# Kernel optimization log

Hardware: AMD Instinct MI355X
Metric: run time of the kernel (lower is better)

The kernel has to match this reference:

```python
import jax, jax.numpy as jnp
import numpy as np

N = 8192      # num nodes
D = 256       # input feature dim (num_embeddings)
F_OUT = 128   # out_channels
B = 4096      # lookup batch size


def setup_inputs() -> dict:
    key = jax.random.key(0)
    k1, k2, k3, k4 = jax.random.split(key, 4)
    x = jax.random.randint(k1, (B,), 0, N)                      # node ids for final lookup
    adj = jax.random.randint(k2, (N, N), 0, 2).astype(jnp.int32)  # dense 0/1 adjacency
    embedding = jax.random.normal(k3, (N, D), dtype=jnp.float32)
    xavier = 1.414 * (6.0 / (D + F_OUT)) ** 0.5
    W = jax.random.uniform(k4, (D, F_OUT), minval=-xavier, maxval=xavier, dtype=jnp.float32)
    return {"x": x, "adj": adj, "embedding": embedding, "W": W}


def reference(x, adj, embedding, W):
    Wh = embedding @ W                                   # [N, F_OUT]
    mask = adj > 0
    maskf = mask.astype(Wh.dtype)
    # per-row neighbor mean of Wh (vectorized form of the python row loop)
    deg = jnp.maximum(jnp.sum(maskf, axis=1), 1.0)       # guard; random adj has deg>0
    neigh_mean = (maskf @ Wh) / deg[:, None]             # [N, F_OUT]
    alpha = jnp.sum(Wh * neigh_mean, axis=1)             # [N], Wh[i] . mean(neighbors)
    e = Wh @ Wh.T + alpha[:, None]                       # similarity + row-wise query term
    att = jax.nn.softmax(jnp.where(mask, e, jnp.asarray(-9e15, e.dtype)), axis=1)
    # dropout is identity in eval mode (p effectively 0)
    h_prime = att @ Wh                                   # [N, F_OUT]
    emb_out = jax.nn.elu(h_prime)                        # concat=True branch
    out = emb_out[x]                                     # F.embedding lookup, [B, F_OUT]
    nrm = jnp.linalg.norm(out, axis=1, keepdims=True)
    return out / jnp.maximum(nrm, 1e-12)                 # F.normalize (L2, eps=1e-12)
```

## Files before the change

kernel.cpp:

```cpp
#include <hip/hip_runtime.h>

#define NN 8192
#define DD 256
#define FF 128
#define BB 4096
#define NSPLIT 16
#define KCHUNK (NN / NSPLIT)
#define NITER (KCHUNK / 64)

typedef unsigned short ushortT;
typedef __attribute__((ext_vector_type(8))) short bf16x8;
typedef __attribute__((ext_vector_type(4))) float f32x4;

__device__ __forceinline__ ushortT f2bf(float f) {
  unsigned u = __float_as_uint(f);
  return (ushortT)((u + 0x7FFFu + ((u >> 16) & 1u)) >> 16);
}
__device__ __forceinline__ float bf2f(ushortT h) {
  return __uint_as_float(((unsigned)h) << 16);
}


__global__ __launch_bounds__(256) void init_kernel(int* flags, int* cnt) {
  int i = blockIdx.x * 256 + threadIdx.x;
  flags[i] = 0;
  if (i == 0) *cnt = 0;
}

__global__ __launch_bounds__(256) void scatter_kernel(const int* __restrict__ x, int* flags) {
  int b = blockIdx.x * 256 + threadIdx.x;
  flags[x[b]] = 1;
}

__global__ __launch_bounds__(256) void compact_kernel(const int* __restrict__ flags, int* cnt,
                                                      int* list, int* slot) {
  int i = blockIdx.x * 256 + threadIdx.x;
  if (flags[i]) {
    int pos = atomicAdd(cnt, 1);
    list[pos] = i;
    slot[i] = pos;
  }
}


__global__ __launch_bounds__(256) void pack_kernel(const int* __restrict__ adj,
                                                   const int* __restrict__ list,
                                                   const int* __restrict__ cntp,
                                                   unsigned* __restrict__ pk) {
  const int s = blockIdx.x >> 2;
  const int kc = (blockIdx.x & 3) * 2048;
  if (s >= *cntp) return;
  const int w = threadIdx.x >> 6, l = threadIdx.x & 63;
  const int* base = adj + (size_t)list[s] * NN + kc + w * 512;
  unsigned long long* dst = (unsigned long long*)(pk + s * 256 + (kc >> 5) + w * 16);
#pragma unroll
  for (int i = 0; i < 8; ++i) {
    unsigned long long b = __ballot(base[i * 64 + l] > 0);
    if (l == 0) dst[i] = b;
  }
}


__global__ __launch_bounds__(256) void wh_kernel(const float* __restrict__ emb,
                                                 const float* __restrict__ W,
                                                 ushortT* __restrict__ Whh,
                                                 ushortT* __restrict__ Whl) {
  __shared__ float Es[32 * 65];
  __shared__ float Ws[64 * 128];
  const int t = threadIdx.x;
  const int r0 = blockIdx.x * 32;
  const int rg = t >> 5;
  const int cg = t & 31;
  float4 acc[4] = {{0,0,0,0},{0,0,0,0},{0,0,0,0},{0,0,0,0}};
  for (int kc = 0; kc < DD; kc += 64) {
    __syncthreads();
    for (int i = 0; i < 8; ++i) {
      int idx = t + 256 * i;
      int r = idx >> 6, k = idx & 63;
      Es[r * 65 + k] = emb[(r0 + r) * DD + kc + k];
    }
    for (int i = 0; i < 8; ++i) {
      int idx = t + 256 * i;
      int kr = idx >> 5, c4 = (idx & 31) * 4;
      *(float4*)&Ws[kr * 128 + c4] = *(const float4*)&W[(kc + kr) * 128 + c4];
    }
    __syncthreads();
    for (int k = 0; k < 64; ++k) {
      float4 b = *(const float4*)&Ws[k * 128 + cg * 4];
#pragma unroll
      for (int i = 0; i < 4; ++i) {
        float a = Es[(rg * 4 + i) * 65 + k];
        acc[i].x += a * b.x; acc[i].y += a * b.y;
        acc[i].z += a * b.z; acc[i].w += a * b.w;
      }
    }
  }
#pragma unroll
  for (int i = 0; i < 4; ++i) {
    int row = r0 + rg * 4 + i;
    float v[4] = {acc[i].x, acc[i].y, acc[i].z, acc[i].w};
    ushort4 hh, ll;
    ushortT* hp = (ushortT*)&hh;
    ushortT* lp = (ushortT*)&ll;
#pragma unroll
    for (int k = 0; k < 4; ++k) {
      ushortT h = f2bf(v[k]);
      hp[k] = h;
      lp[k] = f2bf(v[k] - bf2f(h));
    }
    *(ushort4*)&Whh[row * FF + cg * 4] = hh;
    *(ushort4*)&Whl[row * FF + cg * 4] = ll;
  }
}


__global__ __launch_bounds__(256) void transpose_kernel(const ushortT* __restrict__ A,
                                                        ushortT* __restrict__ At) {
  __shared__ ushortT tile[64 * 72];
  const int t = threadIdx.x;
  const int r0 = (blockIdx.x >> 1) * 64, c0 = (blockIdx.x & 1) * 64;
#pragma unroll
  for (int i = 0; i < 2; ++i) {
    int idx = t + 256 * i;
    int r = idx >> 3, cb = idx & 7;
    *(bf16x8*)&tile[r * 72 + ((cb ^ ((r >> 3) & 7)) * 8)] =
        *(const bf16x8*)&A[(size_t)(r0 + r) * FF + c0 + cb * 8];
  }
  __syncthreads();
#pragma unroll
  for (int i = 0; i < 2; ++i) {
    int idx = t + 256 * i;
    int f = idx >> 3, r8 = idx & 7;
    bf16x8 v;
#pragma unroll
    for (int u = 0; u < 8; ++u) {
      int row = r8 * 8 + u;
      v[u] = (short)tile[row * 72 + (((f >> 3) ^ ((row >> 3) & 7)) * 8) + (f & 7)];
    }
    *(bf16x8*)&At[(size_t)(c0 + f) * NN + r0 + r8 * 8] = v;
  }
}


__global__ __launch_bounds__(256, 3) void attn_kernel(
    const ushortT* __restrict__ Whh, const ushortT* __restrict__ Whl,
    const ushortT* __restrict__ WhT, const unsigned* __restrict__ pk,
    const int* __restrict__ list, const int* __restrict__ cntp,
    float* __restrict__ Opart, float* __restrict__ mpart, float* __restrict__ lpart) {
  __shared__ short Kh[64 * 128];
  __shared__ short Kl[64 * 128];
  __shared__ short Ps[4][16 * 72];
  __shared__ int nid[64];

  const int cnt = *cntp;
  const int qblk = blockIdx.x >> 4, chunk = blockIdx.x & 15;
  const int q0 = qblk * 64;
  if (q0 >= cnt) return;

  const int t = threadIdx.x;
  if (t < 64) nid[t] = list[min(q0 + t, cnt - 1)];
  __syncthreads();

  const int w = t >> 6, l = t & 63, quad = l >> 4, c = l & 15;

  const size_t qr = (size_t)nid[w * 16 + c] * FF;
  bf16x8 qh[4], ql[4];
#pragma unroll
  for (int ks = 0; ks < 4; ++ks) {
    qh[ks] = *(const bf16x8*)(Whh + qr + ks * 32 + quad * 8);
    ql[ks] = *(const bf16x8*)(Whl + qr + ks * 32 + quad * 8);
  }
  int prow[4];
#pragma unroll
  for (int r = 0; r < 4; ++r) prow[r] = min(q0 + w * 16 + quad * 4 + r, cnt - 1);

  float m[4], lr[4];
#pragma unroll
  for (int r = 0; r < 4; ++r) { m[r] = -1e30f; lr[r] = 0.f; }
  f32x4 O[8] = {{0,0,0,0},{0,0,0,0},{0,0,0,0},{0,0,0,0},
                {0,0,0,0},{0,0,0,0},{0,0,0,0},{0,0,0,0}};

  const int kt0 = chunk * KCHUNK;

  bf16x8 sgh[4], sgl[4];
  {
    const ushortT* gh = Whh + (size_t)kt0 * FF;
    const ushortT* gl = Whl + (size_t)kt0 * FF;
#pragma unroll
    for (int i = 0; i < 4; ++i) {
      int idx = t + 256 * i;
      sgh[i] = *(const bf16x8*)(gh + idx * 8);
      sgl[i] = *(const bf16x8*)(gl + idx * 8);
    }
#pragma unroll
    for (int i = 0; i < 4; ++i) {
      int idx = t + 256 * i;
      int r = idx >> 4, cb = idx & 15;
      int off = r * 128 + ((cb ^ (r & 7)) * 8);
      *(bf16x8*)&Kh[off] = sgh[i];
      *(bf16x8*)&Kl[off] = sgl[i];
    }
  }
  __syncthreads();

  for (int it = 0; it < NITER; ++it) {
    const int kt = kt0 + it * 64;

    if (it + 1 < NITER) {
      const ushortT* gh = Whh + (size_t)(kt + 64) * FF;
      const ushortT* gl = Whl + (size_t)(kt + 64) * FF;
#pragma unroll
      for (int i = 0; i < 4; ++i) {
        int idx = t + 256 * i;
        sgh[i] = *(const bf16x8*)(gh + idx * 8);
        sgl[i] = *(const bf16x8*)(gl + idx * 8);
      }
    }

    unsigned mw0[4], mw1[4];
#pragma unroll
    for (int r = 0; r < 4; ++r) {
      uint2 mm = *(const uint2*)(pk + (size_t)prow[r] * 256 + (kt >> 5));
      mw0[r] = mm.x; mw1[r] = mm.y;
    }

    f32x4 sacc[4];
#pragma unroll
    for (int nt = 0; nt < 4; ++nt) {
      const int rb = (nt * 16 + c) * 128;
      f32x4 a = {0, 0, 0, 0};
#pragma unroll
      for (int ks = 0; ks < 4; ++ks) {
        const int off = rb + (((ks * 4 + quad) ^ (c & 7)) * 8);
        bf16x8 bh = *(const bf16x8*)&Kh[off];
        bf16x8 bl = *(const bf16x8*)&Kl[off];
        a = __builtin_amdgcn_mfma_f32_16x16x32_bf16(qh[ks], bh, a, 0, 0, 0);
        a = __builtin_amdgcn_mfma_f32_16x16x32_bf16(ql[ks], bh, a, 0, 0, 0);
        a = __builtin_amdgcn_mfma_f32_16x16x32_bf16(qh[ks], bl, a, 0, 0, 0);
      }
      sacc[nt] = a;
    }

    float rmax[4];
#pragma unroll
    for (int r = 0; r < 4; ++r) {
      float v = -1e30f;
#pragma unroll
      for (int nt = 0; nt < 4; ++nt) {
        unsigned bit = ((nt < 2 ? mw0[r] : mw1[r]) >> ((nt & 1) * 16 + c)) & 1u;
        v = fmaxf(v, bit ? sacc[nt][r] : -1e30f);
      }
      rmax[r] = v;
    }
#pragma unroll
    for (int mk = 1; mk <= 8; mk <<= 1)
#pragma unroll
      for (int r = 0; r < 4; ++r) rmax[r] = fmaxf(rmax[r], __shfl_xor(rmax[r], mk, 16));
    float sc[4], psum[4];
#pragma unroll
    for (int r = 0; r < 4; ++r) {
      float nm = fmaxf(m[r], rmax[r]);
      sc[r] = __expf(m[r] - nm);
      m[r] = nm;
      psum[r] = 0.f;
    }
#pragma unroll
    for (int nt = 0; nt < 4; ++nt)
#pragma unroll
      for (int r = 0; r < 4; ++r) {
        unsigned bit = ((nt < 2 ? mw0[r] : mw1[r]) >> ((nt & 1) * 16 + c)) & 1u;
        float p = bit ? __expf(sacc[nt][r] - m[r]) : 0.f;
        ushortT pb = f2bf(p);
        Ps[w][(quad * 4 + r) * 72 + nt * 16 + c] = (short)pb;
        psum[r] += bf2f(pb);
      }
#pragma unroll
    for (int mk = 1; mk <= 8; mk <<= 1)
#pragma unroll
      for (int r = 0; r < 4; ++r) psum[r] += __shfl_xor(psum[r], mk, 16);
#pragma unroll
    for (int r = 0; r < 4; ++r) lr[r] = lr[r] * sc[r] + psum[r];

#pragma unroll
    for (int ft = 0; ft < 8; ++ft)
#pragma unroll
      for (int r = 0; r < 4; ++r) O[ft][r] *= sc[r];
    bf16x8 pa[2];
#pragma unroll
    for (int ks2 = 0; ks2 < 2; ++ks2)
      pa[ks2] = *(const bf16x8*)&Ps[w][c * 72 + ks2 * 32 + quad * 8];
#pragma unroll
    for (int ft = 0; ft < 8; ++ft) {
      const ushortT* vp = WhT + (size_t)(ft * 16 + c) * NN + kt + quad * 8;
#pragma unroll
      for (int ks2 = 0; ks2 < 2; ++ks2) {
        bf16x8 vb = *(const bf16x8*)(vp + ks2 * 32);
        O[ft] = __builtin_amdgcn_mfma_f32_16x16x32_bf16(pa[ks2], vb, O[ft], 0, 0, 0);
      }
    }

    if (it + 1 < NITER) {
      __syncthreads();
#pragma unroll
      for (int i = 0; i < 4; ++i) {
        int idx = t + 256 * i;
        int r = idx >> 4, cb = idx & 15;
        int off = r * 128 + ((cb ^ (r & 7)) * 8);
        *(bf16x8*)&Kh[off] = sgh[i];
        *(bf16x8*)&Kl[off] = sgl[i];
      }
      __syncthreads();
    }
  }

  float* Op = Opart + (size_t)chunk * 4096 * FF;
#pragma unroll
  for (int ft = 0; ft < 8; ++ft)
#pragma unroll
    for (int r = 0; r < 4; ++r)
      Op[(size_t)(q0 + w * 16 + quad * 4 + r) * FF + ft * 16 + c] = O[ft][r];
  if (c == 0) {
#pragma unroll
    for (int r = 0; r < 4; ++r) {
      mpart[chunk * 4096 + q0 + w * 16 + quad * 4 + r] = m[r];
      lpart[chunk * 4096 + q0 + w * 16 + quad * 4 + r] = lr[r];
    }
  }
}


__global__ __launch_bounds__(128) void combine_kernel(
    const float* __restrict__ Opart, const float* __restrict__ mpart,
    const float* __restrict__ lpart, float* __restrict__ h) {
  const int r = blockIdx.x;
  const int t = threadIdx.x;
  float mstar = -1e30f;
#pragma unroll
  for (int c = 0; c < NSPLIT; ++c) mstar = fmaxf(mstar, mpart[c * 4096 + r]);
  float lstar = 0.f, acc = 0.f;
#pragma unroll
  for (int c = 0; c < NSPLIT; ++c) {
    float wgt = __expf(mpart[c * 4096 + r] - mstar);
    lstar += wgt * lpart[c * 4096 + r];
    acc += wgt * Opart[((size_t)c * 4096 + r) * FF + t];
  }
  float v = acc / fmaxf(lstar, 1e-30f);
  h[r * FF + t] = v > 0.f ? v : expm1f(v);
}


__global__ __launch_bounds__(128) void out_kernel(const int* __restrict__ x,
                                                  const int* __restrict__ slot,
                                                  const float* __restrict__ h,
                                                  float* __restrict__ out) {
  const int b = blockIdx.x, t = threadIdx.x;
  const int s = slot[x[b]];
  float v = h[s * FF + t];
  float ss = v * v;
#pragma unroll
  for (int wd = 1; wd <= 32; wd <<= 1) ss += __shfl_xor(ss, wd);
  __shared__ float red[2];
  if ((t & 63) == 0) red[t >> 6] = ss;
  __syncthreads();
  float tot = red[0] + red[1];
  float scale = 1.f / fmaxf(sqrtf(tot), 1e-12f);
  out[b * FF + t] = v * scale;
}


extern "C" void kernel_launch(void* const* d_in, const int* in_sizes, int n_in,
                              void* d_out, int out_size, void* d_ws, size_t ws_size,
                              hipStream_t stream) {
  const int*   x   = (const int*)d_in[0];
  const int*   adj = (const int*)d_in[1];
  const float* emb = (const float*)d_in[2];
  const float* W   = (const float*)d_in[3];
  float* out = (float*)d_out;

  char* base = (char*)d_ws;
  ushortT* Whh = (ushortT*)(base);
  ushortT* Whl = (ushortT*)(base + 2097152);
  float*   h   = (float*)(base + 2097152);
  ushortT* WhT = (ushortT*)(base + 4194304);
  float* Opart = (float*)(base + 6291456);
  float* mpart = (float*)(base + 39845888);
  float* lpart = (float*)(base + 40108032);
  unsigned* pk = (unsigned*)(base + 40370176);
  int*   flags = (int*)(base + 44564480);
  int*   list  = (int*)(base + 44597248);
  int*   slot  = (int*)(base + 44613632);
  int*   cnt   = (int*)(base + 44646400);
  (void)in_sizes; (void)n_in; (void)out_size; (void)ws_size;

  hipLaunchKernelGGL(init_kernel,      dim3(NN / 256), dim3(256), 0, stream, flags, cnt);
  hipLaunchKernelGGL(scatter_kernel,   dim3(BB / 256), dim3(256), 0, stream, x, flags);
  hipLaunchKernelGGL(compact_kernel,   dim3(NN / 256), dim3(256), 0, stream, flags, cnt, list, slot);
  hipLaunchKernelGGL(pack_kernel,      dim3(4096 * 4), dim3(256), 0, stream, adj, list, cnt, pk);
  hipLaunchKernelGGL(wh_kernel,        dim3(NN / 32),  dim3(256), 0, stream, emb, W, Whh, Whl);
  hipLaunchKernelGGL(transpose_kernel, dim3((NN / 64) * 2), dim3(256), 0, stream, Whh, WhT);
  hipLaunchKernelGGL(attn_kernel,      dim3((BB / 64) * NSPLIT), dim3(256), 0, stream,
                     Whh, Whl, WhT, pk, list, cnt, Opart, mpart, lpart);
  hipLaunchKernelGGL(combine_kernel,   dim3(4096), dim3(128), 0, stream, Opart, mpart, lpart, h);
  hipLaunchKernelGGL(out_kernel,       dim3(BB),   dim3(128), 0, stream, x, slot, h, out);
}
```

Measured before the change: 492.2 us.

## Stage V tile in shared memory with smaller KV block; skip unused combine rows

Halves the KV block from 64 to 32 keys per iteration and stages the transposed value tile (WhT) in swizzled shared memory instead of having every wave read V directly from global memory. All four waves now reuse one shared V tile, which cuts redundant global traffic in the P·V product. The price is twice as many iterations and barriers, plus extra LDS. Separately, combine_kernel exits early for rows beyond the unique-node count.

```diff
diff --git a/kernel.cpp b/kernel.cpp
--- a/kernel.cpp
+++ b/kernel.cpp
@@ -6,7 +6,8 @@
 #define BB 4096
 #define NSPLIT 16
 #define KCHUNK (NN / NSPLIT)
-#define NITER (KCHUNK / 64)
+#define KVBLK 32
+#define NITER (KCHUNK / KVBLK)
 
 typedef unsigned short ushortT;
 typedef __attribute__((ext_vector_type(8))) short bf16x8;
@@ -147,9 +148,10 @@
     const ushortT* __restrict__ WhT, const unsigned* __restrict__ pk,
     const int* __restrict__ list, const int* __restrict__ cntp,
     float* __restrict__ Opart, float* __restrict__ mpart, float* __restrict__ lpart) {
-  __shared__ short Kh[64 * 128];
-  __shared__ short Kl[64 * 128];
-  __shared__ short Ps[4][16 * 72];
+  __shared__ short Kh[KVBLK * 128];
+  __shared__ short Kl[KVBLK * 128];
+  __shared__ short Vs[128 * KVBLK];
+  __shared__ short Ps[4][16 * 40];
   __shared__ int nid[64];
 
   const int cnt = *cntp;
@@ -182,51 +184,54 @@
 
   const int kt0 = chunk * KCHUNK;
 
-  bf16x8 sgh[4], sgl[4];
+  bf16x8 sgh[2], sgl[2], sgv[2];
   {
     const ushortT* gh = Whh + (size_t)kt0 * FF;
     const ushortT* gl = Whl + (size_t)kt0 * FF;
 #pragma unroll
-    for (int i = 0; i < 4; ++i) {
+    for (int i = 0; i < 2; ++i) {
       int idx = t + 256 * i;
       sgh[i] = *(const bf16x8*)(gh + idx * 8);
       sgl[i] = *(const bf16x8*)(gl + idx * 8);
-    }
-#pragma unroll
-    for (int i = 0; i < 4; ++i) {
+      int vr = idx >> 2, vcb = idx & 3;
+      sgv[i] = *(const bf16x8*)(WhT + (size_t)vr * NN + kt0 + vcb * 8);
+    }
+#pragma unroll
+    for (int i = 0; i < 2; ++i) {
       int idx = t + 256 * i;
       int r = idx >> 4, cb = idx & 15;
       int off = r * 128 + ((cb ^ (r & 7)) * 8);
       *(bf16x8*)&Kh[off] = sgh[i];
       *(bf16x8*)&Kl[off] = sgl[i];
+      int vr = idx >> 2, vcb = idx & 3;
+      *(bf16x8*)&Vs[vr * KVBLK + ((vcb ^ (vr & 3)) * 8)] = sgv[i];
     }
   }
   __syncthreads();
 
   for (int it = 0; it < NITER; ++it) {
-    const int kt = kt0 + it * 64;
+    const int kt = kt0 + it * KVBLK;
 
     if (it + 1 < NITER) {
-      const ushortT* gh = Whh + (size_t)(kt + 64) * FF;
-      const ushortT* gl = Whl + (size_t)(kt + 64) * FF;
-#pragma unroll
-      for (int i = 0; i < 4; ++i) {
+      const ushortT* gh = Whh + (size_t)(kt + KVBLK) * FF;
+      const ushortT* gl = Whl + (size_t)(kt + KVBLK) * FF;
+#pragma unroll
+      for (int i = 0; i < 2; ++i) {
         int idx = t + 256 * i;
         sgh[i] = *(const bf16x8*)(gh + idx * 8);
         sgl[i] = *(const bf16x8*)(gl + idx * 8);
-      }
-    }
-
-    unsigned mw0[4], mw1[4];
-#pragma unroll
-    for (int r = 0; r < 4; ++r) {
-      uint2 mm = *(const uint2*)(pk + (size_t)prow[r] * 256 + (kt >> 5));
-      mw0[r] = mm.x; mw1[r] = mm.y;
-    }
-
-    f32x4 sacc[4];
-#pragma unroll
-    for (int nt = 0; nt < 4; ++nt) {
+        int vr = idx >> 2, vcb = idx & 3;
+        sgv[i] = *(const bf16x8*)(WhT + (size_t)vr * NN + (kt + KVBLK) + vcb * 8);
+      }
+    }
+
+    unsigned m32[4];
+#pragma unroll
+    for (int r = 0; r < 4; ++r) m32[r] = pk[(size_t)prow[r] * 256 + (kt >> 5)];
+
+    f32x4 sacc[2];
+#pragma unroll
+    for (int nt = 0; nt < 2; ++nt) {
       const int rb = (nt * 16 + c) * 128;
       f32x4 a = {0, 0, 0, 0};
 #pragma unroll
@@ -246,8 +251,8 @@
     for (int r = 0; r < 4; ++r) {
       float v = -1e30f;
 #pragma unroll
-      for (int nt = 0; nt < 4; ++nt) {
-        unsigned bit = ((nt < 2 ? mw0[r] : mw1[r]) >> ((nt & 1) * 16 + c)) & 1u;
+      for (int nt = 0; nt < 2; ++nt) {
+        unsigned bit = (m32[r] >> (nt * 16 + c)) & 1u;
         v = fmaxf(v, bit ? sacc[nt][r] : -1e30f);
       }
       rmax[r] = v;
@@ -265,13 +270,13 @@
       psum[r] = 0.f;
     }
 #pragma unroll
-    for (int nt = 0; nt < 4; ++nt)
+    for (int nt = 0; nt < 2; ++nt)
 #pragma unroll
       for (int r = 0; r < 4; ++r) {
-        unsigned bit = ((nt < 2 ? mw0[r] : mw1[r]) >> ((nt & 1) * 16 + c)) & 1u;
+        unsigned bit = (m32[r] >> (nt * 16 + c)) & 1u;
         float p = bit ? __expf(sacc[nt][r] - m[r]) : 0.f;
         ushortT pb = f2bf(p);
-        Ps[w][(quad * 4 + r) * 72 + nt * 16 + c] = (short)pb;
+        Ps[w][(quad * 4 + r) * 40 + nt * 16 + c] = (short)pb;
         psum[r] += bf2f(pb);
       }
 #pragma unroll
@@ -285,29 +290,26 @@
     for (int ft = 0; ft < 8; ++ft)
 #pragma unroll
       for (int r = 0; r < 4; ++r) O[ft][r] *= sc[r];
-    bf16x8 pa[2];
-#pragma unroll
-    for (int ks2 = 0; ks2 < 2; ++ks2)
-      pa[ks2] = *(const bf16x8*)&Ps[w][c * 72 + ks2 * 32 + quad * 8];
+    bf16x8 pa = *(const bf16x8*)&Ps[w][c * 40 + quad * 8];
 #pragma unroll
     for (int ft = 0; ft < 8; ++ft) {
-      const ushortT* vp = WhT + (size_t)(ft * 16 + c) * NN + kt + quad * 8;
-#pragma unroll
-      for (int ks2 = 0; ks2 < 2; ++ks2) {
-        bf16x8 vb = *(const bf16x8*)(vp + ks2 * 32);
-        O[ft] = __builtin_amdgcn_mfma_f32_16x16x32_bf16(pa[ks2], vb, O[ft], 0, 0, 0);
-      }
+      const int vrow = ft * 16 + c;
+      const int voff = vrow * KVBLK + ((quad ^ (vrow & 3)) * 8);
+      bf16x8 vb = *(const bf16x8*)&Vs[voff];
+      O[ft] = __builtin_amdgcn_mfma_f32_16x16x32_bf16(pa, vb, O[ft], 0, 0, 0);
     }
 
     if (it + 1 < NITER) {
       __syncthreads();
 #pragma unroll
-      for (int i = 0; i < 4; ++i) {
+      for (int i = 0; i < 2; ++i) {
         int idx = t + 256 * i;
         int r = idx >> 4, cb = idx & 15;
         int off = r * 128 + ((cb ^ (r & 7)) * 8);
         *(bf16x8*)&Kh[off] = sgh[i];
         *(bf16x8*)&Kl[off] = sgl[i];
+        int vr = idx >> 2, vcb = idx & 3;
+        *(bf16x8*)&Vs[vr * KVBLK + ((vcb ^ (vr & 3)) * 8)] = sgv[i];
       }
       __syncthreads();
     }
@@ -331,8 +333,10 @@
 
 __global__ __launch_bounds__(128) void combine_kernel(
     const float* __restrict__ Opart, const float* __restrict__ mpart,
-    const float* __restrict__ lpart, float* __restrict__ h) {
+    const float* __restrict__ lpart, const int* __restrict__ cntp,
+    float* __restrict__ h) {
   const int r = blockIdx.x;
+  if (r >= *cntp) return;
   const int t = threadIdx.x;
   float mstar = -1e30f;
 #pragma unroll
@@ -400,6 +404,6 @@
   hipLaunchKernelGGL(transpose_kernel, dim3((NN / 64) * 2), dim3(256), 0, stream, Whh, WhT);
   hipLaunchKernelGGL(attn_kernel,      dim3((BB / 64) * NSPLIT), dim3(256), 0, stream,
                      Whh, Whl, WhT, pk, list, cnt, Opart, mpart, lpart);
-  hipLaunchKernelGGL(combine_kernel,   dim3(4096), dim3(128), 0, stream, Opart, mpart, lpart, h);
+  hipLaunchKernelGGL(combine_kernel,   dim3(4096), dim3(128), 0, stream, Opart, mpart, lpart, cnt, h);
   hipLaunchKernelGGL(out_kernel,       dim3(BB),   dim3(128), 0, stream, x, slot, h, out);
 }
```

Result: faster. 453.8 us (-7.8%).
